# Performance work log

Hardware: AMD Instinct MI355X
Metric: run time of the kernel (lower is better)

Reference implementation:

```python
import jax, jax.numpy as jnp
import numpy as np

B, N, M = 16, 2048, 2048


def setup_inputs() -> dict:
    key = jax.random.key(0)
    k1, k2, k3 = jax.random.split(key, 3)
    pred_dsmat = jax.random.uniform(k1, (B, N, M), dtype=jnp.float32)
    # valid sizes: src_ns <= tgt_ns so a permutation GT exists for every valid row
    src_ns = jax.random.randint(k2, (B,), 1024, 1537, dtype=jnp.int32)
    tgt_ns = jax.random.randint(k3, (B,), 1537, 2049, dtype=jnp.int32)
    # gt_perm: identity permutation restricted to the valid region (one 1 per valid row)
    i = jnp.arange(N)[:, None]
    j = jnp.arange(M)[None, :]
    eye = (i == j).astype(jnp.float32)  # [N, M]
    row_mask = (jnp.arange(N)[None, :] < src_ns[:, None]).astype(jnp.float32)  # [B, N]
    gt_perm = eye[None, :, :] * row_mask[:, :, None]  # [B, N, M]
    return {"pred_dsmat": pred_dsmat, "gt_perm": gt_perm,
            "src_ns": src_ns, "tgt_ns": tgt_ns, "beta_value": 0.1}


def reference(pred_dsmat, gt_perm, src_ns, tgt_ns, beta_value):
    Bn, Nn, Mn = pred_dsmat.shape
    row_mask = jnp.arange(Nn)[None, :] < src_ns[:, None]   # [B, N] bool
    col_mask = jnp.arange(Mn)[None, :] < tgt_ns[:, None]   # [B, M] bool
    mask = row_mask[:, :, None] & col_mask[:, None, :]     # [B, N, M]

    pred = jnp.clip(pred_dsmat, 0.0, 1.0) * mask
    gt = gt_perm * mask

    gt_pred = pred * gt                      # gt-selected predicted values
    row_gt = gt_pred.sum(axis=2)             # [B, N] per-row GT value
    col_gt = gt_pred.sum(axis=1)             # [B, M] per-col GT value
    row_cnt = gt.sum(axis=2)                 # [B, N] #GT matches per row
    col_cnt = gt.sum(axis=1)                 # [B, M] #GT matches per col

    # attention masks: entries >= (gt value - beta), restricted to valid region
    att_src = ((pred >= row_gt[:, :, None] - beta_value) & mask) * row_cnt[:, :, None]
    att_tgt = ((pred >= col_gt[:, None, :] - beta_value) & mask) * col_cnt[:, None, :]

    src_neg = jnp.sum(((att_src - gt) * pred) ** 2, axis=2)  # [B, N]
    src_pos = jnp.sum(gt_pred ** 2, axis=2)                  # [B, N]
    tgt_neg = jnp.sum(((att_tgt - gt) * pred) ** 2, axis=1)  # [B, M]

    # sum of tgt_neg over the GT-matched column of each row == dot with column counts
    corr = jnp.einsum('bm,bm->b', tgt_neg, col_cnt)          # [B]

    denom = 1.0 + src_neg + corr[:, None]                    # [B, N]
    num = jnp.where(row_mask, src_pos, 1.0)
    den = jnp.where(row_mask, denom, 1.0)
    loss = -0.5 * jnp.sum(jnp.log(num / den) * row_mask)
    n_sum = src_ns.sum().astype(pred.dtype)
    return loss / n_sum
```

## Files before the change

### kernel.cpp

```cpp
#include <hip/hip_runtime.h>

#define B_ 16
#define N_ 2048
#define M_ 2048
#define ROWS 64
#define WROWS 16

__device__ __forceinline__ float wave_sum(float v) {
#pragma unroll
    for (int off = 32; off >= 1; off >>= 1) v += __shfl_xor(v, off);
    return v;
}

extern "C" __global__ __launch_bounds__(256) void k_pass1(
    const float* __restrict__ pred, const float* __restrict__ gt,
    const int* __restrict__ src_ns, const int* __restrict__ tgt_ns,
    float* __restrict__ row_gt, float* __restrict__ row_cnt,
    float* __restrict__ col_gt, float* __restrict__ col_cnt)
{
    const int b = blockIdx.y;
    const int src = src_ns[b];
    const int band = blockIdx.x;
    if (band * ROWS >= src) return;
    const int tgt = tgt_ns[b];
    const int wave = threadIdx.x >> 6, lane = threadIdx.x & 63;
    const int base = b * (N_ * M_);

    float4 acg[8], accn[8];
#pragma unroll
    for (int j = 0; j < 8; ++j) { acg[j] = make_float4(0,0,0,0); accn[j] = make_float4(0,0,0,0); }

    const int row0 = band * ROWS + wave * WROWS;
    for (int r = 0; r < WROWS; ++r) {
        const int n = row0 + r;
        if (n >= src) break;
        const float4* prow = (const float4*)(pred + base + n * M_);
        const float4* grow = (const float4*)(gt + base + n * M_);
        float rg = 0.f, rc = 0.f;
#pragma unroll
        for (int j = 0; j < 8; ++j) {
            const int m4 = j * 64 + lane;
            const float4 p4 = prow[m4];
            const float4 g4 = grow[m4];
            const int mb = m4 * 4;
#define P1C(K, MB) do { \
    const bool ok = (mb + K) < tgt; \
    float p = fminf(fmaxf(p4.MB, 0.f), 1.f); p = ok ? p : 0.f; \
    const float g = ok ? g4.MB : 0.f; \
    const float gp = p * g; \
    rg += gp; rc += g; \
    acg[j].MB += gp; accn[j].MB += g; \
} while (0)
            P1C(0, x); P1C(1, y); P1C(2, z); P1C(3, w);
#undef P1C
        }
        rg = wave_sum(rg); rc = wave_sum(rc);
        if (lane == 0) { row_gt[b * N_ + n] = rg; row_cnt[b * N_ + n] = rc; }
    }

    __shared__ float4 s_cg[M_ / 4];
    __shared__ float4 s_cc[M_ / 4];
    for (int i = threadIdx.x; i < M_ / 4; i += 256) {
        s_cg[i] = make_float4(0,0,0,0);
        s_cc[i] = make_float4(0,0,0,0);
    }
    __syncthreads();
    for (int w = 0; w < 4; ++w) {
        if (wave == w) {
#pragma unroll
            for (int j = 0; j < 8; ++j) {
                const int i = j * 64 + lane;
                float4 v = s_cg[i];
                v.x += acg[j].x; v.y += acg[j].y; v.z += acg[j].z; v.w += acg[j].w;
                s_cg[i] = v;
                float4 u = s_cc[i];
                u.x += accn[j].x; u.y += accn[j].y; u.z += accn[j].z; u.w += accn[j].w;
                s_cc[i] = u;
            }
        }
        __syncthreads();
    }
    const float* fcg = (const float*)s_cg;
    const float* fcc = (const float*)s_cc;
    for (int i = threadIdx.x; i < M_; i += 256) {
        atomicAdd(&col_gt[b * M_ + i], fcg[i]);
        atomicAdd(&col_cnt[b * M_ + i], fcc[i]);
    }
}

extern "C" __global__ __launch_bounds__(256) void k_pass2(
    const float* __restrict__ pred, const float* __restrict__ gt,
    const int* __restrict__ src_ns, const int* __restrict__ tgt_ns,
    const float* __restrict__ beta_p,
    const float* __restrict__ row_gt, const float* __restrict__ row_cnt,
    const float* __restrict__ col_gt, const float* __restrict__ col_cnt,
    float* __restrict__ src_neg, float* __restrict__ src_pos,
    float* __restrict__ tgt_neg)
{
    const int b = blockIdx.y;
    const int src = src_ns[b];
    const int band = blockIdx.x;
    if (band * ROWS >= src) return;
    const int tgt = tgt_ns[b];
    const float beta = beta_p[0];
    const int wave = threadIdx.x >> 6, lane = threadIdx.x & 63;
    const int base = b * (N_ * M_);

    float4 cg[8], cc[8], tn[8];
    const float4* cg4 = (const float4*)(col_gt + b * M_);
    const float4* cc4 = (const float4*)(col_cnt + b * M_);
#pragma unroll
    for (int j = 0; j < 8; ++j) {
        cg[j] = cg4[j * 64 + lane];
        cc[j] = cc4[j * 64 + lane];
        tn[j] = make_float4(0,0,0,0);
    }

    const int row0 = band * ROWS + wave * WROWS;
    for (int r = 0; r < WROWS; ++r) {
        const int n = row0 + r;
        if (n >= src) break;
        const float rg = row_gt[b * N_ + n];
        const float rc = row_cnt[b * N_ + n];
        const float rth = rg - beta;
        const float4* prow = (const float4*)(pred + base + n * M_);
        const float4* grow = (const float4*)(gt + base + n * M_);
        float sneg = 0.f, spos = 0.f;
#pragma unroll
        for (int j = 0; j < 8; ++j) {
            const int m4 = j * 64 + lane;
            const float4 p4 = prow[m4];
            const float4 g4 = grow[m4];
            const int mb = m4 * 4;
#define P2C(K, MB) do { \
    const bool ok = (mb + K) < tgt; \
    float p = fminf(fmaxf(p4.MB, 0.f), 1.f); p = ok ? p : 0.f; \
    const float g = ok ? g4.MB : 0.f; \
    const float gp = p * g; \
    const float as = (ok && (p >= rth)) ? rc : 0.f; \
    const float ds = (as - g) * p; \
    sneg += ds * ds; spos += gp * gp; \
    const float at = (ok && (p >= cg[j].MB - beta)) ? cc[j].MB : 0.f; \
    const float dt = (at - g) * p; \
    tn[j].MB += dt * dt; \
} while (0)
            P2C(0, x); P2C(1, y); P2C(2, z); P2C(3, w);
#undef P2C
        }
        sneg = wave_sum(sneg); spos = wave_sum(spos);
        if (lane == 0) { src_neg[b * N_ + n] = sneg; src_pos[b * N_ + n] = spos; }
    }

    __shared__ float4 s_tn[M_ / 4];
    for (int i = threadIdx.x; i < M_ / 4; i += 256) s_tn[i] = make_float4(0,0,0,0);
    __syncthreads();
    for (int w = 0; w < 4; ++w) {
        if (wave == w) {
#pragma unroll
            for (int j = 0; j < 8; ++j) {
                const int i = j * 64 + lane;
                float4 v = s_tn[i];
                v.x += tn[j].x; v.y += tn[j].y; v.z += tn[j].z; v.w += tn[j].w;
                s_tn[i] = v;
            }
        }
        __syncthreads();
    }
    const float* ftn = (const float*)s_tn;
    for (int i = threadIdx.x; i < M_; i += 256)
        atomicAdd(&tgt_neg[b * M_ + i], ftn[i]);
}

extern "C" __global__ __launch_bounds__(256) void k_final(
    const float* __restrict__ src_neg, const float* __restrict__ src_pos,
    const float* __restrict__ tgt_neg, const float* __restrict__ col_cnt,
    const int* __restrict__ src_ns, float* __restrict__ out)
{
    const int b = blockIdx.x;
    const int wave = threadIdx.x >> 6, lane = threadIdx.x & 63;
    __shared__ float sredc[4];
    __shared__ float sredl[4];

    float c = 0.f;
    for (int i = threadIdx.x; i < M_; i += 256)
        c += tgt_neg[b * M_ + i] * col_cnt[b * M_ + i];
    c = wave_sum(c);
    if (lane == 0) sredc[wave] = c;
    __syncthreads();
    const float corr = sredc[0] + sredc[1] + sredc[2] + sredc[3];

    const int src = src_ns[b];
    float ls = 0.f;
    for (int n = threadIdx.x; n < src; n += 256) {
        const float sp = src_pos[b * N_ + n];
        const float sn = src_neg[b * N_ + n];
        ls += logf(sp) - logf(1.f + sn + corr);
    }
    ls = wave_sum(ls);
    if (lane == 0) sredl[wave] = ls;
    __syncthreads();
    if (threadIdx.x == 0) {
        const float total = sredl[0] + sredl[1] + sredl[2] + sredl[3];
        float nsum = 0.f;
        for (int i = 0; i < B_; ++i) nsum += (float)src_ns[i];
        atomicAdd(out, -0.5f * total / nsum);
    }
}

extern "C" void kernel_launch(void* const* d_in, const int* in_sizes, int n_in,
                              void* d_out, int out_size, void* d_ws, size_t ws_size,
                              hipStream_t stream)
{
    const float* pred   = (const float*)d_in[0];
    const float* gtp    = (const float*)d_in[1];
    const int*   src_ns = (const int*)d_in[2];
    const int*   tgt_ns = (const int*)d_in[3];
    const float* beta   = (const float*)d_in[4];
    float* out = (float*)d_out;
    float* ws  = (float*)d_ws;

    float* row_gt  = ws;
    float* row_cnt = row_gt  + B_ * N_;
    float* col_gt  = row_cnt + B_ * N_;
    float* col_cnt = col_gt  + B_ * M_;
    float* src_neg = col_cnt + B_ * M_;
    float* src_pos = src_neg + B_ * N_;
    float* tgt_neg = src_pos + B_ * N_;

    const size_t zero_bytes = (size_t)(4 * B_ * N_ + 3 * B_ * M_) * sizeof(float);
    hipMemsetAsync(d_ws, 0, zero_bytes, stream);
    hipMemsetAsync(d_out, 0, sizeof(float), stream);

    dim3 grid(N_ / ROWS, B_);
    k_pass1<<<grid, 256, 0, stream>>>(pred, gtp, src_ns, tgt_ns,
                                      row_gt, row_cnt, col_gt, col_cnt);
    k_pass2<<<grid, 256, 0, stream>>>(pred, gtp, src_ns, tgt_ns, beta,
                                      row_gt, row_cnt, col_gt, col_cnt,
                                      src_neg, src_pos, tgt_neg);
    k_final<<<B_, 256, 0, stream>>>(src_neg, src_pos, tgt_neg, col_cnt, src_ns, out);
}
```

Measured before the change: 558.2 us.

## Fuse row terms into pass1 and skip gt reads in pass2 via sparse GT list

Pass1 now computes src_neg/src_pos from register-held row data right after the row reductions, so pass2 no longer has to recompute them. Pass1 also records each row's nonzero GT entries, up to two per row, in a small sparse list. If no row overflows, pass2 reads only pred and patches the few GT positions with atomic corrections, avoiding a full read of the dense gt tensor. Rows per block are halved. The trade-off is per-nonzero atomics in pass1, a dense fallback kept behind a flag, and higher register use from caching the row in pass1.

```diff
diff --git a/kernel.cpp b/kernel.cpp
--- a/kernel.cpp
+++ b/kernel.cpp
@@ -3,8 +3,9 @@
 #define B_ 16
 #define N_ 2048
 #define M_ 2048
-#define ROWS 64
-#define WROWS 16
+#define ROWS 32
+#define WROWS 8
+#define KCAP 2
 
 __device__ __forceinline__ float wave_sum(float v) {
 #pragma unroll
@@ -15,14 +16,18 @@
 extern "C" __global__ __launch_bounds__(256) void k_pass1(
     const float* __restrict__ pred, const float* __restrict__ gt,
     const int* __restrict__ src_ns, const int* __restrict__ tgt_ns,
-    float* __restrict__ row_gt, float* __restrict__ row_cnt,
-    float* __restrict__ col_gt, float* __restrict__ col_cnt)
+    const float* __restrict__ beta_p,
+    float* __restrict__ col_gt, float* __restrict__ col_cnt,
+    float* __restrict__ src_neg, float* __restrict__ src_pos,
+    int* __restrict__ nnz, int* __restrict__ ent_col,
+    float* __restrict__ ent_val, int* flag)
 {
     const int b = blockIdx.y;
     const int src = src_ns[b];
     const int band = blockIdx.x;
     if (band * ROWS >= src) return;
     const int tgt = tgt_ns[b];
+    const float beta = beta_p[0];
     const int wave = threadIdx.x >> 6, lane = threadIdx.x & 63;
     const int base = b * (N_ * M_);
 
@@ -34,28 +39,53 @@
     for (int r = 0; r < WROWS; ++r) {
         const int n = row0 + r;
         if (n >= src) break;
+        const int ri = b * N_ + n;
         const float4* prow = (const float4*)(pred + base + n * M_);
         const float4* grow = (const float4*)(gt + base + n * M_);
         float rg = 0.f, rc = 0.f;
+        float4 pr[8], gr[8];
 #pragma unroll
         for (int j = 0; j < 8; ++j) {
             const int m4 = j * 64 + lane;
-            const float4 p4 = prow[m4];
-            const float4 g4 = grow[m4];
+            float4 p4 = prow[m4];
+            float4 g4 = grow[m4];
             const int mb = m4 * 4;
-#define P1C(K, MB) do { \
-    const bool ok = (mb + K) < tgt; \
+#define P1C(KK, MB) do { \
+    const int c = mb + KK; \
+    const bool ok = c < tgt; \
     float p = fminf(fmaxf(p4.MB, 0.f), 1.f); p = ok ? p : 0.f; \
-    const float g = ok ? g4.MB : 0.f; \
-    const float gp = p * g; \
-    rg += gp; rc += g; \
-    acg[j].MB += gp; accn[j].MB += g; \
+    const float gv = ok ? g4.MB : 0.f; \
+    const float gp = p * gv; \
+    rg += gp; rc += gv; \
+    acg[j].MB += gp; accn[j].MB += gv; \
+    p4.MB = p; g4.MB = gv; \
+    if (gv != 0.f) { \
+        const int slot = atomicAdd(&nnz[ri], 1); \
+        if (slot < KCAP) { ent_col[ri * KCAP + slot] = c; ent_val[ri * KCAP + slot] = gv; } \
+        else *flag = 1; \
+    } \
 } while (0)
             P1C(0, x); P1C(1, y); P1C(2, z); P1C(3, w);
 #undef P1C
+            pr[j] = p4; gr[j] = g4;
         }
         rg = wave_sum(rg); rc = wave_sum(rc);
-        if (lane == 0) { row_gt[b * N_ + n] = rg; row_cnt[b * N_ + n] = rc; }
+        const float rth = rg - beta;
+        float sneg = 0.f, spos = 0.f;
+#pragma unroll
+        for (int j = 0; j < 8; ++j) {
+#define P1S(MB) do { \
+    const float p = pr[j].MB; const float gv = gr[j].MB; \
+    const float as = (p >= rth) ? rc : 0.f; \
+    const float ds = (as - gv) * p; \
+    sneg += ds * ds; \
+    const float gp = gv * p; spos += gp * gp; \
+} while (0)
+            P1S(x); P1S(y); P1S(z); P1S(w);
+#undef P1S
+        }
+        sneg = wave_sum(sneg); spos = wave_sum(spos);
+        if (lane == 0) { src_neg[ri] = sneg; src_pos[ri] = spos; }
     }
 
     __shared__ float4 s_cg[M_ / 4];
@@ -92,9 +122,9 @@
     const float* __restrict__ pred, const float* __restrict__ gt,
     const int* __restrict__ src_ns, const int* __restrict__ tgt_ns,
     const float* __restrict__ beta_p,
-    const float* __restrict__ row_gt, const float* __restrict__ row_cnt,
     const float* __restrict__ col_gt, const float* __restrict__ col_cnt,
-    float* __restrict__ src_neg, float* __restrict__ src_pos,
+    const int* __restrict__ nnz, const int* __restrict__ ent_col,
+    const float* __restrict__ ent_val, const int* flag,
     float* __restrict__ tgt_neg)
 {
     const int b = blockIdx.y;
@@ -105,6 +135,7 @@
     const float beta = beta_p[0];
     const int wave = threadIdx.x >> 6, lane = threadIdx.x & 63;
     const int base = b * (N_ * M_);
+    const bool dense = (*flag != 0);
 
     float4 cg[8], cc[8], tn[8];
     const float4* cg4 = (const float4*)(col_gt + b * M_);
@@ -117,38 +148,66 @@
     }
 
     const int row0 = band * ROWS + wave * WROWS;
-    for (int r = 0; r < WROWS; ++r) {
-        const int n = row0 + r;
-        if (n >= src) break;
-        const float rg = row_gt[b * N_ + n];
-        const float rc = row_cnt[b * N_ + n];
-        const float rth = rg - beta;
-        const float4* prow = (const float4*)(pred + base + n * M_);
-        const float4* grow = (const float4*)(gt + base + n * M_);
-        float sneg = 0.f, spos = 0.f;
-#pragma unroll
-        for (int j = 0; j < 8; ++j) {
-            const int m4 = j * 64 + lane;
-            const float4 p4 = prow[m4];
-            const float4 g4 = grow[m4];
-            const int mb = m4 * 4;
-#define P2C(K, MB) do { \
-    const bool ok = (mb + K) < tgt; \
+    if (!dense) {
+        for (int r = 0; r < WROWS; ++r) {
+            const int n = row0 + r;
+            if (n >= src) break;
+            const float4* prow = (const float4*)(pred + base + n * M_);
+#pragma unroll
+            for (int j = 0; j < 8; ++j) {
+                const int m4 = j * 64 + lane;
+                const float4 p4 = prow[m4];
+                const int mb = m4 * 4;
+#define P2S(KK, MB) do { \
+    const bool ok = (mb + KK) < tgt; \
     float p = fminf(fmaxf(p4.MB, 0.f), 1.f); p = ok ? p : 0.f; \
-    const float g = ok ? g4.MB : 0.f; \
-    const float gp = p * g; \
-    const float as = (ok && (p >= rth)) ? rc : 0.f; \
-    const float ds = (as - g) * p; \
-    sneg += ds * ds; spos += gp * gp; \
+    const float at = (p >= cg[j].MB - beta) ? cc[j].MB : 0.f; \
+    const float d = at * p; \
+    tn[j].MB += d * d; \
+} while (0)
+                P2S(0, x); P2S(1, y); P2S(2, z); P2S(3, w);
+#undef P2S
+            }
+            const int ri = b * N_ + n;
+            const int nn = nnz[ri];
+            if (nn > 0 && lane == 0) {
+                const int ne = nn < KCAP ? nn : KCAP;
+                for (int s = 0; s < ne; ++s) {
+                    const int c = ent_col[ri * KCAP + s];
+                    const float gv = ent_val[ri * KCAP + s];
+                    float pv = pred[base + n * M_ + c];
+                    pv = fminf(fmaxf(pv, 0.f), 1.f);
+                    const float at = (pv >= col_gt[b * M_ + c] - beta) ? col_cnt[b * M_ + c] : 0.f;
+                    const float d0 = at * pv;
+                    const float d1 = (at - gv) * pv;
+                    atomicAdd(&tgt_neg[b * M_ + c], d1 * d1 - d0 * d0);
+                }
+            }
+        }
+    } else {
+        for (int r = 0; r < WROWS; ++r) {
+            const int n = row0 + r;
+            if (n >= src) break;
+            const float4* prow = (const float4*)(pred + base + n * M_);
+            const float4* grow = (const float4*)(gt + base + n * M_);
+#pragma unroll
+            for (int j = 0; j < 8; ++j) {
+                const int m4 = j * 64 + lane;
+                const float4 p4 = prow[m4];
+                const float4 g4 = grow[m4];
+                const int mb = m4 * 4;
+#define P2D(KK, MB) do { \
+    const bool ok = (mb + KK) < tgt; \
+    float p = fminf(fmaxf(p4.MB, 0.f), 1.f); p = ok ? p : 0.f; \
+    const float gv = ok ? g4.MB : 0.f; \
     const float at = (ok && (p >= cg[j].MB - beta)) ? cc[j].MB : 0.f; \
-    const float dt = (at - g) * p; \
+    const float dt = (at - gv) * p; \
     tn[j].MB += dt * dt; \
 } while (0)
-            P2C(0, x); P2C(1, y); P2C(2, z); P2C(3, w);
-#undef P2C
-        }
-        sneg = wave_sum(sneg); spos = wave_sum(spos);
-        if (lane == 0) { src_neg[b * N_ + n] = sneg; src_pos[b * N_ + n] = spos; }
+                P2D(0, x); P2D(1, y); P2D(2, z); P2D(3, w);
+#undef P2D
+            }
+        }
     }
 
     __shared__ float4 s_tn[M_ / 4];
@@ -219,23 +278,26 @@
     float* out = (float*)d_out;
     float* ws  = (float*)d_ws;
 
-    float* row_gt  = ws;
-    float* row_cnt = row_gt  + B_ * N_;
-    float* col_gt  = row_cnt + B_ * N_;
+    float* col_gt  = ws;
     float* col_cnt = col_gt  + B_ * M_;
-    float* src_neg = col_cnt + B_ * M_;
+    float* tgt_neg = col_cnt + B_ * M_;
+    int*   nnz     = (int*)(tgt_neg + B_ * M_);
+    int*   flag    = nnz + B_ * N_;
+    float* src_neg = (float*)(flag + 1);
     float* src_pos = src_neg + B_ * N_;
-    float* tgt_neg = src_pos + B_ * N_;
-
-    const size_t zero_bytes = (size_t)(4 * B_ * N_ + 3 * B_ * M_) * sizeof(float);
+    int*   ent_col = (int*)(src_pos + B_ * N_);
+    float* ent_val = (float*)(ent_col + B_ * N_ * KCAP);
+
+    const size_t zero_bytes = (size_t)(3 * B_ * M_ + B_ * N_ + 1) * sizeof(float);
     hipMemsetAsync(d_ws, 0, zero_bytes, stream);
     hipMemsetAsync(d_out, 0, sizeof(float), stream);
 
     dim3 grid(N_ / ROWS, B_);
-    k_pass1<<<grid, 256, 0, stream>>>(pred, gtp, src_ns, tgt_ns,
-                                      row_gt, row_cnt, col_gt, col_cnt);
+    k_pass1<<<grid, 256, 0, stream>>>(pred, gtp, src_ns, tgt_ns, beta,
+                                      col_gt, col_cnt, src_neg, src_pos,
+                                      nnz, ent_col, ent_val, flag);
     k_pass2<<<grid, 256, 0, stream>>>(pred, gtp, src_ns, tgt_ns, beta,
-                                      row_gt, row_cnt, col_gt, col_cnt,
-                                      src_neg, src_pos, tgt_neg);
+                                      col_gt, col_cnt, nnz, ent_col, ent_val, flag,
+                                      tgt_neg);
     k_final<<<B_, 256, 0, stream>>>(src_neg, src_pos, tgt_neg, col_cnt, src_ns, out);
 }
```

Result: no change. 567.2 us (+1.6%).
